# Kernel optimization log

Hardware: AMD Instinct MI355X
Metric: run time of the kernel (lower is better)

## Reference

```python
import jax, jax.numpy as jnp
import numpy as np

N = 262144   # number of samples
C = 16       # GMM components
D = 64       # feature dim


def setup_inputs() -> dict:
    key = jax.random.key(0)
    k1, k2, k3, k4 = jax.random.split(key, 4)
    inputs = jax.random.normal(k1, (N, D), dtype=jnp.float32)
    # SPD inverse covariances, as produced by inverting fitted GMM covariances
    R = jax.random.normal(k2, (C, D, D), dtype=jnp.float32)
    covariances_inv = jnp.einsum('cij,ckj->cik', R, R) / D + 0.1 * jnp.eye(D, dtype=jnp.float32)
    means = jax.random.normal(k3, (C, D), dtype=jnp.float32)
    w = jax.random.uniform(k4, (C,), dtype=jnp.float32, minval=0.1, maxval=1.0)
    weights = w / jnp.sum(w)  # mixture weights sum to 1
    return {"inputs": inputs, "covariances_inv": covariances_inv,
            "means": means, "weights": weights}


def reference(inputs, covariances_inv, means, weights):
    # Mahalanobis quadratic form per component: d[n,c] = (x_n - m_c)^T Sigma_c^{-1} (x_n - m_c)
    centered = inputs[:, None, :] - means[None, :, :]                # [N, C, D]
    distances_sqr = jnp.einsum('ncd,cde,nce->nc', centered, covariances_inv, centered)  # [N, C]
    # score_n = prod_c d[n,c] ** w_c
    score = jnp.prod(distances_sqr ** weights[None, :], axis=1)      # [N]
    return score
```

## Files before the change

kernel.cpp:

```cpp
#include <hip/hip_runtime.h>

typedef __attribute__((ext_vector_type(4))) float f32x4;
typedef __attribute__((ext_vector_type(8))) short bf16x8;

__device__ __forceinline__ short f2bf(float f) {
    union { float f; unsigned u; } v; v.f = f;
    unsigned u = v.u;
    u += 0x7FFFu + ((u >> 16) & 1u);
    return (short)(u >> 16);
}

__device__ __forceinline__ float hw_log2(float x) { return __builtin_amdgcn_logf(x); }
__device__ __forceinline__ float hw_exp2(float x) { return __builtin_amdgcn_exp2f(x); }

__global__ void gmm_prep(const float* __restrict__ Ainv,
                         const float* __restrict__ means,
                         short* __restrict__ AbP,
                         float* __restrict__ biasP,
                         float* __restrict__ kscal) {
    int c = blockIdx.x;
    int j = threadIdx.x;
    const float* A = Ainv + c * 4096;
    const float* m = means + c * 64;
    float b = 0.f;
    #pragma unroll 8
    for (int k = 0; k < 64; ++k) b += A[j * 64 + k] * m[k];
    float km = m[j] * b;
    #pragma unroll
    for (int off = 32; off >= 1; off >>= 1) km += __shfl_xor(km, off, 64);
    if (j == 0) kscal[c] = km;

    int rt = j >> 4, qh = (j >> 2) & 3, r = j & 3;
    int pj = (rt < 2) ? (8 * qh + 4 * rt + r) : (32 + 8 * qh + 4 * (rt - 2) + r);
    biasP[c * 64 + j] = -2.0f * __shfl(b, pj, 64);

    const float* Arow = A + pj * 64;
    short* dst = AbP + c * 4096 + j * 64;
    #pragma unroll 8
    for (int k = 0; k < 64; ++k) dst[k] = f2bf(Arow[k]);
}

__global__ __launch_bounds__(256) void gmm_main(
    const float* __restrict__ X,
    const float* __restrict__ weights,
    const short* __restrict__ AbP,
    const float* __restrict__ biasP,
    const float* __restrict__ kscal,
    float* __restrict__ out) {

    __shared__ short sAb[2][64 * 72];
    __shared__ float sBias[16 * 64];
    __shared__ float sKW[32];

    const int tid = threadIdx.x;
    const int lane = tid & 63;
    const int w = tid >> 6;
    const int q = lane >> 4;
    const int ln = lane & 15;

    ((f32x4*)sBias)[tid] = ((const f32x4*)biasP)[tid];
    if (tid < 16) { sKW[tid] = kscal[tid]; sKW[16 + tid] = weights[tid]; }
    const int srow = tid >> 2;
    const int scol = (tid & 3) * 16;
    {
        const int4* src = (const int4*)(AbP + tid * 16);
        int4 a0 = src[0], a1 = src[1];
        int4* dst = (int4*)&sAb[0][srow * 72 + scol];
        dst[0] = a0; dst[1] = a1;
    }

    const int nbase = blockIdx.x * 128 + w * 32;
    f32x4 xv[2][2][2];
    bf16x8 bfr[2][2];
    #pragma unroll
    for (int t = 0; t < 2; ++t) {
        const float* xrow = X + (size_t)(nbase + t * 16 + ln) * 64 + q * 8;
        #pragma unroll
        for (int kc = 0; kc < 2; ++kc) {
            f32x4 xa = *(const f32x4*)(xrow + kc * 32);
            f32x4 xb = *(const f32x4*)(xrow + kc * 32 + 4);
            xv[t][kc][0] = xa; xv[t][kc][1] = xb;
            bf16x8 s;
            #pragma unroll
            for (int i = 0; i < 4; ++i) { s[i] = f2bf(xa[i]); s[4 + i] = f2bf(xb[i]); }
            bfr[t][kc] = s;
        }
    }
    __syncthreads();

    float slog[2] = {0.f, 0.f};

    for (int c = 0; c < 16; ++c) {
        const int buf = c & 1;
        int4 p0, p1;
        if (c < 15) {
            const int4* src = (const int4*)(AbP + (c + 1) * 4096 + tid * 16);
            p0 = src[0]; p1 = src[1];
        }

        bf16x8 af[4][2];
        f32x4 bias[4];
        #pragma unroll
        for (int rt = 0; rt < 4; ++rt) {
            #pragma unroll
            for (int kc = 0; kc < 2; ++kc)
                af[rt][kc] = *(const bf16x8*)&sAb[buf][(rt * 16 + ln) * 72 + kc * 32 + q * 8];
            bias[rt] = *(const f32x4*)&sBias[c * 64 + rt * 16 + q * 4];
        }

        #pragma unroll
        for (int t = 0; t < 2; ++t) {
            float dp = 0.f;
            #pragma unroll
            for (int rt = 0; rt < 4; ++rt) {
                f32x4 acc = __builtin_amdgcn_mfma_f32_16x16x32_bf16(
                    af[rt][0], bfr[t][0], bias[rt], 0, 0, 0);
                acc = __builtin_amdgcn_mfma_f32_16x16x32_bf16(
                    af[rt][1], bfr[t][1], acc, 0, 0, 0);
                f32x4 xm = xv[t][rt >> 1][rt & 1];
                dp += acc[0] * xm[0] + acc[1] * xm[1]
                    + acc[2] * xm[2] + acc[3] * xm[3];
            }
            dp += __shfl_xor(dp, 16, 64);
            dp += __shfl_xor(dp, 32, 64);
            float d = dp + sKW[c];
            d = fmaxf(d, 1e-30f);
            slog[t] += sKW[16 + c] * hw_log2(d);
        }

        if (c < 15) {
            int4* dst = (int4*)&sAb[buf ^ 1][srow * 72 + scol];
            dst[0] = p0; dst[1] = p1;
        }
        __syncthreads();
    }

    if (q == 0) {
        out[nbase + ln]      = hw_exp2(slog[0]);
        out[nbase + 16 + ln] = hw_exp2(slog[1]);
    }
}

extern "C" void kernel_launch(void* const* d_in, const int* in_sizes, int n_in,
                              void* d_out, int out_size, void* d_ws, size_t ws_size,
                              hipStream_t stream) {
    const float* X       = (const float*)d_in[0];
    const float* Ainv    = (const float*)d_in[1];
    const float* means   = (const float*)d_in[2];
    const float* weights = (const float*)d_in[3];
    float* out = (float*)d_out;
    const int N = in_sizes[0] / 64;

    short* AbP   = (short*)d_ws;
    float* biasP = (float*)((char*)d_ws + 131072);
    float* kscal = (float*)((char*)d_ws + 135168);

    gmm_prep<<<dim3(16), dim3(64), 0, stream>>>(Ainv, means, AbP, biasP, kscal);
    gmm_main<<<dim3(N / 128), dim3(256), 0, stream>>>(X, weights, AbP, biasP, kscal, out);
}
```

Baseline: 140.0 us.

## Split components across waves with register-resident matrices and streamed sample tiles

Each wave now holds the bf16 inverse-covariance fragments of four components in registers and streams 16-sample tiles through a 32-iteration loop with a next-tile prefetch. The shared-memory double buffer and the per-component block barrier go away. The linear bias term moves into a separate small MFMA against a packed -2·Σ⁻¹m vector. Per-wave partial log-scores are summed through shared memory every 8 tiles, and the prep kernel is rewritten to stage the matrix in LDS. The cost is heavy register pressure (64 bf16x8 fragments), far fewer blocks, and the bias now in bf16 rather than fp32, which lowers precision.

```diff
diff --git a/kernel.cpp b/kernel.cpp
--- a/kernel.cpp
+++ b/kernel.cpp
@@ -10,134 +10,174 @@
     return (short)(u >> 16);
 }
 
-__device__ __forceinline__ float hw_log2(float x) { return __builtin_amdgcn_logf(x); }
-__device__ __forceinline__ float hw_exp2(float x) { return __builtin_amdgcn_exp2f(x); }
+__device__ __forceinline__ int pack_bf2(float a, float b) {
+    union { float f; unsigned u; } ua, ub; ua.f = a; ub.f = b;
+    unsigned x = ua.u + 0x8000u, y = ub.u + 0x8000u;
+    return (int)__builtin_amdgcn_perm(y, x, 0x07060302u);
+}
 
 __global__ void gmm_prep(const float* __restrict__ Ainv,
                          const float* __restrict__ means,
                          short* __restrict__ AbP,
-                         float* __restrict__ biasP,
+                         short* __restrict__ Bneg2,
                          float* __restrict__ kscal) {
-    int c = blockIdx.x;
-    int j = threadIdx.x;
+    __shared__ float sA[64 * 68];
+    __shared__ float sm[64];
+    __shared__ float sb[64];
+    const int c = blockIdx.x, t = threadIdx.x;
     const float* A = Ainv + c * 4096;
-    const float* m = means + c * 64;
-    float b = 0.f;
-    #pragma unroll 8
-    for (int k = 0; k < 64; ++k) b += A[j * 64 + k] * m[k];
-    float km = m[j] * b;
-    #pragma unroll
-    for (int off = 32; off >= 1; off >>= 1) km += __shfl_xor(km, off, 64);
-    if (j == 0) kscal[c] = km;
-
-    int rt = j >> 4, qh = (j >> 2) & 3, r = j & 3;
-    int pj = (rt < 2) ? (8 * qh + 4 * rt + r) : (32 + 8 * qh + 4 * (rt - 2) + r);
-    biasP[c * 64 + j] = -2.0f * __shfl(b, pj, 64);
-
-    const float* Arow = A + pj * 64;
-    short* dst = AbP + c * 4096 + j * 64;
-    #pragma unroll 8
-    for (int k = 0; k < 64; ++k) dst[k] = f2bf(Arow[k]);
-}
-
-__global__ __launch_bounds__(256) void gmm_main(
+    #pragma unroll
+    for (int i = 0; i < 4; ++i) {
+        int flat = i * 1024 + t * 4;
+        int r = flat >> 6, col = flat & 63;
+        *(f32x4*)&sA[r * 68 + col] = *(const f32x4*)(A + flat);
+    }
+    if (t < 64) sm[t] = means[c * 64 + t];
+    __syncthreads();
+    {
+        int j = t >> 2, seg = t & 3;
+        float p = 0.f;
+        #pragma unroll
+        for (int k = 0; k < 16; ++k) p += sA[j * 68 + seg * 16 + k] * sm[seg * 16 + k];
+        p += __shfl_xor(p, 1, 64); p += __shfl_xor(p, 2, 64);
+        if ((t & 3) == 0) sb[j] = p;
+    }
+    __syncthreads();
+    if (t < 64) {
+        float km = sm[t] * sb[t];
+        #pragma unroll
+        for (int off = 32; off >= 1; off >>= 1) km += __shfl_xor(km, off, 64);
+        if (t == 0) kscal[c] = km;
+        Bneg2[c * 64 + t] = f2bf(-2.f * sb[t]);
+    }
+    {
+        int p_ = t >> 2, kq = (t & 3) * 16;
+        int rt = p_ >> 4, qh = (p_ >> 2) & 3, r = p_ & 3;
+        int pj = (rt >> 1) * 32 + 8 * qh + 4 * (rt & 1) + r;
+        bf16x8 v0, v1;
+        #pragma unroll
+        for (int i = 0; i < 8; ++i) {
+            v0[i] = f2bf(sA[pj * 68 + kq + i]);
+            v1[i] = f2bf(sA[pj * 68 + kq + 8 + i]);
+        }
+        *(bf16x8*)(AbP + c * 4096 + p_ * 64 + kq)     = v0;
+        *(bf16x8*)(AbP + c * 4096 + p_ * 64 + kq + 8) = v1;
+    }
+}
+
+__global__ __launch_bounds__(256, 2) void gmm_main(
     const float* __restrict__ X,
     const float* __restrict__ weights,
     const short* __restrict__ AbP,
-    const float* __restrict__ biasP,
+    const short* __restrict__ Bneg2,
     const float* __restrict__ kscal,
     float* __restrict__ out) {
 
-    __shared__ short sAb[2][64 * 72];
-    __shared__ float sBias[16 * 64];
-    __shared__ float sKW[32];
+    __shared__ float sPart[8 * 4 * 16];
 
     const int tid = threadIdx.x;
-    const int lane = tid & 63;
-    const int w = tid >> 6;
-    const int q = lane >> 4;
-    const int ln = lane & 15;
-
-    ((f32x4*)sBias)[tid] = ((const f32x4*)biasP)[tid];
-    if (tid < 16) { sKW[tid] = kscal[tid]; sKW[16 + tid] = weights[tid]; }
-    const int srow = tid >> 2;
-    const int scol = (tid & 3) * 16;
-    {
-        const int4* src = (const int4*)(AbP + tid * 16);
-        int4 a0 = src[0], a1 = src[1];
-        int4* dst = (int4*)&sAb[0][srow * 72 + scol];
-        dst[0] = a0; dst[1] = a1;
-    }
-
-    const int nbase = blockIdx.x * 128 + w * 32;
-    f32x4 xv[2][2][2];
-    bf16x8 bfr[2][2];
-    #pragma unroll
-    for (int t = 0; t < 2; ++t) {
-        const float* xrow = X + (size_t)(nbase + t * 16 + ln) * 64 + q * 8;
-        #pragma unroll
-        for (int kc = 0; kc < 2; ++kc) {
-            f32x4 xa = *(const f32x4*)(xrow + kc * 32);
-            f32x4 xb = *(const f32x4*)(xrow + kc * 32 + 4);
-            xv[t][kc][0] = xa; xv[t][kc][1] = xb;
-            bf16x8 s;
-            #pragma unroll
-            for (int i = 0; i < 4; ++i) { s[i] = f2bf(xa[i]); s[4 + i] = f2bf(xb[i]); }
-            bfr[t][kc] = s;
-        }
-    }
-    __syncthreads();
-
-    float slog[2] = {0.f, 0.f};
-
-    for (int c = 0; c < 16; ++c) {
-        const int buf = c & 1;
-        int4 p0, p1;
-        if (c < 15) {
-            const int4* src = (const int4*)(AbP + (c + 1) * 4096 + tid * 16);
-            p0 = src[0]; p1 = src[1];
-        }
-
-        bf16x8 af[4][2];
-        f32x4 bias[4];
-        #pragma unroll
-        for (int rt = 0; rt < 4; ++rt) {
+    const int lane = tid & 63, w = tid >> 6;
+    const int q = lane >> 4, ln = lane & 15;
+
+    bf16x8 af[4][4][2];
+    const short* Aw = AbP + (w * 4) * 4096 + ln * 64 + q * 8;
+    #pragma unroll
+    for (int c4 = 0; c4 < 4; ++c4)
+        #pragma unroll
+        for (int rt = 0; rt < 4; ++rt)
             #pragma unroll
             for (int kc = 0; kc < 2; ++kc)
-                af[rt][kc] = *(const bf16x8*)&sAb[buf][(rt * 16 + ln) * 72 + kc * 32 + q * 8];
-            bias[rt] = *(const f32x4*)&sBias[c * 64 + rt * 16 + q * 4];
-        }
-
-        #pragma unroll
-        for (int t = 0; t < 2; ++t) {
+                af[c4][rt][kc] = *(const bf16x8*)(Aw + c4 * 4096 + rt * 1024 + kc * 32);
+
+    bf16x8 ab[2];
+    {
+        bf16x8 z;
+        #pragma unroll
+        for (int i = 0; i < 8; ++i) z[i] = 0;
+        ab[0] = z; ab[1] = z;
+        if (ln < 4) {
+            ab[0] = *(const bf16x8*)(Bneg2 + (w * 4 + ln) * 64 + q * 8);
+            ab[1] = *(const bf16x8*)(Bneg2 + (w * 4 + ln) * 64 + 32 + q * 8);
+        }
+    }
+    float kw[4], wc[4];
+    #pragma unroll
+    for (int c4 = 0; c4 < 4; ++c4) { kw[c4] = kscal[w * 4 + c4]; wc[c4] = weights[w * 4 + c4]; }
+
+    const int base = blockIdx.x * 512;
+    const float* xp = X + (size_t)(base + ln) * 64 + q * 8;
+    f32x4 xc[2][2];
+    #pragma unroll
+    for (int kc = 0; kc < 2; ++kc) {
+        xc[kc][0] = *(const f32x4*)(xp + kc * 32);
+        xc[kc][1] = *(const f32x4*)(xp + kc * 32 + 4);
+    }
+
+    const f32x4 zero4 = {0.f, 0.f, 0.f, 0.f};
+
+    #pragma unroll 1
+    for (int t = 0; t < 32; ++t) {
+        const float* xnp = xp + 1024;
+        f32x4 xn[2][2];
+        if (t < 31) {
+            #pragma unroll
+            for (int kc = 0; kc < 2; ++kc) {
+                xn[kc][0] = *(const f32x4*)(xnp + kc * 32);
+                xn[kc][1] = *(const f32x4*)(xnp + kc * 32 + 4);
+            }
+        }
+
+        bf16x8 bfr[2];
+        #pragma unroll
+        for (int kc = 0; kc < 2; ++kc) {
+            union { int i[4]; bf16x8 v; } u;
+            u.i[0] = pack_bf2(xc[kc][0][0], xc[kc][0][1]);
+            u.i[1] = pack_bf2(xc[kc][0][2], xc[kc][0][3]);
+            u.i[2] = pack_bf2(xc[kc][1][0], xc[kc][1][1]);
+            u.i[3] = pack_bf2(xc[kc][1][2], xc[kc][1][3]);
+            bfr[kc] = u.v;
+        }
+
+        f32x4 bacc = __builtin_amdgcn_mfma_f32_16x16x32_bf16(ab[0], bfr[0], zero4, 0, 0, 0);
+        bacc = __builtin_amdgcn_mfma_f32_16x16x32_bf16(ab[1], bfr[1], bacc, 0, 0, 0);
+
+        float slog = 0.f;
+        #pragma unroll
+        for (int c4 = 0; c4 < 4; ++c4) {
             float dp = 0.f;
             #pragma unroll
             for (int rt = 0; rt < 4; ++rt) {
                 f32x4 acc = __builtin_amdgcn_mfma_f32_16x16x32_bf16(
-                    af[rt][0], bfr[t][0], bias[rt], 0, 0, 0);
+                    af[c4][rt][0], bfr[0], zero4, 0, 0, 0);
                 acc = __builtin_amdgcn_mfma_f32_16x16x32_bf16(
-                    af[rt][1], bfr[t][1], acc, 0, 0, 0);
-                f32x4 xm = xv[t][rt >> 1][rt & 1];
+                    af[c4][rt][1], bfr[1], acc, 0, 0, 0);
+                f32x4 xm = xc[rt >> 1][rt & 1];
                 dp += acc[0] * xm[0] + acc[1] * xm[1]
                     + acc[2] * xm[2] + acc[3] * xm[3];
             }
             dp += __shfl_xor(dp, 16, 64);
             dp += __shfl_xor(dp, 32, 64);
-            float d = dp + sKW[c];
-            d = fmaxf(d, 1e-30f);
-            slog[t] += sKW[16 + c] * hw_log2(d);
-        }
-
-        if (c < 15) {
-            int4* dst = (int4*)&sAb[buf ^ 1][srow * 72 + scol];
-            dst[0] = p0; dst[1] = p1;
-        }
-        __syncthreads();
-    }
-
-    if (q == 0) {
-        out[nbase + ln]      = hw_exp2(slog[0]);
-        out[nbase + 16 + ln] = hw_exp2(slog[1]);
+            if (q == 0) {
+                float d = dp + bacc[c4] + kw[c4];
+                d = fmaxf(d, 1e-30f);
+                slog += wc[c4] * __builtin_amdgcn_logf(d);
+            }
+        }
+        if (q == 0) sPart[(t & 7) * 64 + w * 16 + ln] = slog;
+
+        if ((t & 7) == 7) {
+            __syncthreads();
+            if (tid < 128) {
+                int s = tid, o = (s >> 4) * 64 + (s & 15);
+                float v = sPart[o] + sPart[o + 16] + sPart[o + 32] + sPart[o + 48];
+                out[base + (t >> 3) * 128 + s] = __builtin_amdgcn_exp2f(v);
+            }
+            __syncthreads();
+        }
+
+        xp = xnp;
+        #pragma unroll
+        for (int kc = 0; kc < 2; ++kc) { xc[kc][0] = xn[kc][0]; xc[kc][1] = xn[kc][1]; }
     }
 }
 
@@ -152,9 +192,9 @@
     const int N = in_sizes[0] / 64;
 
     short* AbP   = (short*)d_ws;
-    float* biasP = (float*)((char*)d_ws + 131072);
-    float* kscal = (float*)((char*)d_ws + 135168);
-
-    gmm_prep<<<dim3(16), dim3(64), 0, stream>>>(Ainv, means, AbP, biasP, kscal);
-    gmm_main<<<dim3(N / 128), dim3(256), 0, stream>>>(X, weights, AbP, biasP, kscal, out);
-}
+    short* Bneg2 = (short*)((char*)d_ws + 131072);
+    float* kscal = (float*)((char*)d_ws + 133120);
+
+    gmm_prep<<<dim3(16), dim3(256), 0, stream>>>(Ainv, means, AbP, Bneg2, kscal);
+    gmm_main<<<dim3(N / 512), dim3(256), 0, stream>>>(X, weights, AbP, Bneg2, kscal, out);
+}
```

After: 144.9 us. 3.5% more time.
